# Optimization experiments

Hardware: AMD Instinct MI355X
Metric: run time of the kernel (lower is better)

## Reference

```python
import jax, jax.numpy as jnp
import numpy as np


def setup_inputs() -> dict:
    key = jax.random.key(0)
    k1, k2 = jax.random.split(key)
    B, N1, N2, D = 256, 32, 32, 512
    ner_j = jax.random.normal(k1, (B, N1, D), dtype=jnp.float32)
    face_j = jax.random.normal(k2, (B, N2, D), dtype=jnp.float32)
    return {"face_j": face_j, "ner_j": ner_j}


def reference(face_j, ner_j):
    # torch.matmul(ner_j.unsqueeze(1), face_j.permute(0,2,1)) broadcasts to the
    # pairwise score tensor: scores[b, c, n, f] = <ner_j[b, n], face_j[c, f]>
    scores = jnp.einsum('bnd,cfd->bcnf', ner_j, face_j)  # (B, B, N1, N2)
    # mean over num_spans2 then mean over num_spans1 (sum + div in original)
    logits = scores.mean(axis=-1).mean(axis=-1)           # (B, B)
    # cross_entropy(logits, targets=arange(B)) with mean reduction
    logp = jax.nn.log_softmax(logits, axis=-1)
    diag = jnp.diagonal(logp)                             # logp[b, b]
    return -jnp.mean(diag)
```

## Files before the change

kernel.cpp:

```cpp
#include <hip/hip_runtime.h>
#include <hip/hip_bf16.h>

#define BB 256
#define NN 32
#define DD 512
#define ROWS 2
#define KSPLIT 4

static __device__ inline unsigned f2bf(float x) {
  union { float f; unsigned u; } a; a.f = x;
  unsigned r = a.u + 0x7fff + ((a.u >> 16) & 1);
  return r >> 16;
}

__global__ __launch_bounds__(256) void reduce_sums(
    const float* __restrict__ ner, const float* __restrict__ face,
    float* __restrict__ u, unsigned* __restrict__ vTp, float* __restrict__ out) {
  int idx = blockIdx.x * 256 + threadIdx.x;
  if (idx == 0) out[0] = 0.0f;
  const int half = BB * DD / 4;
  bool is_ner = idx < half;
  int j = is_ner ? idx : idx - half;
  int row = j >> 7;
  int d4  = j & 127;
  const float* src = is_ner ? ner : face;
  const float4* p = (const float4*)(src + (size_t)row * NN * DD) + d4;
  float4 s = make_float4(0.f, 0.f, 0.f, 0.f);
#pragma unroll
  for (int n = 0; n < NN; ++n) {
    float4 x = p[n * (DD / 4)];
    s.x += x.x; s.y += x.y; s.z += x.z; s.w += x.w;
  }
  if (is_ner) {
    ((float4*)(u + (size_t)row * DD))[d4] = s;
  } else {
    int dp0 = 2 * d4;
    vTp[(size_t)dp0 * BB + row]       = (f2bf(s.y) << 16) | f2bf(s.x);
    vTp[(size_t)(dp0 + 1) * BB + row] = (f2bf(s.w) << 16) | f2bf(s.z);
  }
}

__global__ __launch_bounds__(1024) void row_lse_bf16(
    const float* __restrict__ u, const unsigned* __restrict__ vTp,
    float* __restrict__ out) {
  const int b0 = blockIdx.x * ROWS;
  const int t = threadIdx.x;
  const int c = t & 255;
  const int k = t >> 8;
  __shared__ float us[ROWS * DD];
  __shared__ float ls[KSPLIT][ROWS][BB];
  __shared__ float lg[ROWS][BB];
  __shared__ float wsum[ROWS];

  if (t < ROWS * DD / 4)
    ((float4*)us)[t] = ((const float4*)(u + (size_t)b0 * DD))[t];
  __syncthreads();

  float a0l = 0.f, a0h = 0.f, a1l = 0.f, a1h = 0.f;
  const unsigned* p = vTp + (size_t)(k * (DD / 2 / KSPLIT)) * BB + c;
  const float* u0 = us + k * (DD / KSPLIT);
  const float* u1 = us + DD + k * (DD / KSPLIT);
#pragma unroll 8
  for (int i = 0; i < DD / 2 / KSPLIT; ++i) {
    unsigned w = p[(size_t)i * BB];
    float vlo = __uint_as_float(w << 16);
    float vhi = __uint_as_float(w & 0xffff0000u);
    a0l = fmaf(u0[2 * i],     vlo, a0l);
    a0h = fmaf(u0[2 * i + 1], vhi, a0h);
    a1l = fmaf(u1[2 * i],     vlo, a1l);
    a1h = fmaf(u1[2 * i + 1], vhi, a1h);
  }
  ls[k][0][c] = a0l + a0h;
  ls[k][1][c] = a1l + a1h;
  __syncthreads();

  const float sc = 1.f / (NN * NN);
  if (t < ROWS * BB) {
    int cc = t & 255, r = t >> 8;
    lg[r][cc] = (ls[0][r][cc] + ls[1][r][cc] + ls[2][r][cc] + ls[3][r][cc]) * sc;
  }
  __syncthreads();

  const int wv = t >> 6, lane = t & 63;
  if (wv < ROWS) {
    float x0 = lg[wv][lane];
    float x1 = lg[wv][lane + 64];
    float x2 = lg[wv][lane + 128];
    float x3 = lg[wv][lane + 192];
    float m = fmaxf(fmaxf(x0, x1), fmaxf(x2, x3));
#pragma unroll
    for (int off = 32; off > 0; off >>= 1) m = fmaxf(m, __shfl_xor(m, off, 64));
    float e = __expf(x0 - m) + __expf(x1 - m) + __expf(x2 - m) + __expf(x3 - m);
#pragma unroll
    for (int off = 32; off > 0; off >>= 1) e += __shfl_xor(e, off, 64);
    if (lane == 0) wsum[wv] = lg[wv][b0 + wv] - (m + __logf(e));
  }
  __syncthreads();
  if (t == 0) atomicAdd(out, -(wsum[0] + wsum[1]) * (1.f / BB));
}

extern "C" void kernel_launch(void* const* d_in, const int* in_sizes, int n_in,
                              void* d_out, int out_size, void* d_ws, size_t ws_size,
                              hipStream_t stream) {
  const float* face = (const float*)d_in[0];
  const float* ner  = (const float*)d_in[1];
  float* u = (float*)d_ws;
  unsigned* vTp = (unsigned*)(u + (size_t)BB * DD);
  float* out = (float*)d_out;

  const int total_threads = 2 * BB * DD / 4;
  reduce_sums<<<total_threads / 256, 256, 0, stream>>>(ner, face, u, vTp, out);
  row_lse_bf16<<<BB / ROWS, 1024, 0, stream>>>(u, vTp, out);
}
```

Before: 80.00 us.

## Fuse span-sum and logsumexp kernels into one cooperative launch with grid sync

Merges the span-reduction kernel and the row log-softmax kernel into a single cooperative kernel of 256 blocks of 512 threads, with a grid-wide barrier between the phases. This removes one kernel launch and the dependency gap between them. The first phase now reduces float2 pairs per thread instead of float4, and the second phase computes one row per block with a 2-way K split instead of two rows per block with a 4-way split. The cost is the grid-sync overhead and less memory-level parallelism per thread in the reduction phase.

```diff
diff --git a/kernel.cpp b/kernel.cpp
--- a/kernel.cpp
+++ b/kernel.cpp
@@ -1,11 +1,12 @@
 #include <hip/hip_runtime.h>
-#include <hip/hip_bf16.h>
+#include <hip/hip_cooperative_groups.h>
+
+namespace cg = cooperative_groups;
 
 #define BB 256
 #define NN 32
 #define DD 512
-#define ROWS 2
-#define KSPLIT 4
+#define D2 (DD / 2)
 
 static __device__ inline unsigned f2bf(float x) {
   union { float f; unsigned u; } a; a.f = x;
@@ -13,90 +14,75 @@
   return r >> 16;
 }
 
-__global__ __launch_bounds__(256) void reduce_sums(
+__global__ __launch_bounds__(512) void fused_nce(
     const float* __restrict__ ner, const float* __restrict__ face,
-    float* __restrict__ u, unsigned* __restrict__ vTp, float* __restrict__ out) {
-  int idx = blockIdx.x * 256 + threadIdx.x;
-  if (idx == 0) out[0] = 0.0f;
-  const int half = BB * DD / 4;
-  bool is_ner = idx < half;
-  int j = is_ner ? idx : idx - half;
-  int row = j >> 7;
-  int d4  = j & 127;
-  const float* src = is_ner ? ner : face;
-  const float4* p = (const float4*)(src + (size_t)row * NN * DD) + d4;
-  float4 s = make_float4(0.f, 0.f, 0.f, 0.f);
+    float* __restrict__ u, unsigned* __restrict__ vTp,
+    float* __restrict__ out) {
+  const int t = threadIdx.x;
+  const int idx = blockIdx.x * 512 + t;
+
+  if (idx == 0) atomicExch(out, 0.0f);
+
+  {
+    const bool is_ner = idx < (BB * D2);
+    const int j = is_ner ? idx : idx - BB * D2;
+    const int row = j >> 8;
+    const int d2 = j & 255;
+    const float2* p =
+        (const float2*)(is_ner ? ner : face) + (size_t)row * (NN * D2) + d2;
+    float sx = 0.f, sy = 0.f;
 #pragma unroll
-  for (int n = 0; n < NN; ++n) {
-    float4 x = p[n * (DD / 4)];
-    s.x += x.x; s.y += x.y; s.z += x.z; s.w += x.w;
+    for (int n = 0; n < NN; ++n) {
+      float2 x = p[(size_t)n * D2];
+      sx += x.x; sy += x.y;
+    }
+    if (is_ner) {
+      ((float2*)u)[(size_t)row * D2 + d2] = make_float2(sx, sy);
+    } else {
+      vTp[(size_t)d2 * BB + row] = (f2bf(sy) << 16) | f2bf(sx);
+    }
   }
-  if (is_ner) {
-    ((float4*)(u + (size_t)row * DD))[d4] = s;
-  } else {
-    int dp0 = 2 * d4;
-    vTp[(size_t)dp0 * BB + row]       = (f2bf(s.y) << 16) | f2bf(s.x);
-    vTp[(size_t)(dp0 + 1) * BB + row] = (f2bf(s.w) << 16) | f2bf(s.z);
-  }
-}
 
-__global__ __launch_bounds__(1024) void row_lse_bf16(
-    const float* __restrict__ u, const unsigned* __restrict__ vTp,
-    float* __restrict__ out) {
-  const int b0 = blockIdx.x * ROWS;
-  const int t = threadIdx.x;
+  __threadfence();
+  cg::this_grid().sync();
+
+  const int b = blockIdx.x;
   const int c = t & 255;
   const int k = t >> 8;
-  __shared__ float us[ROWS * DD];
-  __shared__ float ls[KSPLIT][ROWS][BB];
-  __shared__ float lg[ROWS][BB];
-  __shared__ float wsum[ROWS];
+  __shared__ float us[DD];
+  __shared__ float ls[2][BB];
+  __shared__ float lg[BB];
 
-  if (t < ROWS * DD / 4)
-    ((float4*)us)[t] = ((const float4*)(u + (size_t)b0 * DD))[t];
+  us[t] = u[(size_t)b * DD + t];
   __syncthreads();
 
-  float a0l = 0.f, a0h = 0.f, a1l = 0.f, a1h = 0.f;
-  const unsigned* p = vTp + (size_t)(k * (DD / 2 / KSPLIT)) * BB + c;
-  const float* u0 = us + k * (DD / KSPLIT);
-  const float* u1 = us + DD + k * (DD / KSPLIT);
+  float al = 0.f, ah = 0.f;
+  const unsigned* p = vTp + (size_t)(k * (D2 / 2)) * BB + c;
+  const float* ub = us + k * (DD / 2);
 #pragma unroll 8
-  for (int i = 0; i < DD / 2 / KSPLIT; ++i) {
+  for (int i = 0; i < D2 / 2; ++i) {
     unsigned w = p[(size_t)i * BB];
     float vlo = __uint_as_float(w << 16);
     float vhi = __uint_as_float(w & 0xffff0000u);
-    a0l = fmaf(u0[2 * i],     vlo, a0l);
-    a0h = fmaf(u0[2 * i + 1], vhi, a0h);
-    a1l = fmaf(u1[2 * i],     vlo, a1l);
-    a1h = fmaf(u1[2 * i + 1], vhi, a1h);
+    al = fmaf(ub[2 * i],     vlo, al);
+    ah = fmaf(ub[2 * i + 1], vhi, ah);
   }
-  ls[k][0][c] = a0l + a0h;
-  ls[k][1][c] = a1l + a1h;
+  ls[k][c] = al + ah;
   __syncthreads();
 
-  const float sc = 1.f / (NN * NN);
-  if (t < ROWS * BB) {
-    int cc = t & 255, r = t >> 8;
-    lg[r][cc] = (ls[0][r][cc] + ls[1][r][cc] + ls[2][r][cc] + ls[3][r][cc]) * sc;
-  }
+  if (t < BB) lg[t] = (ls[0][t] + ls[1][t]) * (1.f / (NN * NN));
   __syncthreads();
 
-  const int wv = t >> 6, lane = t & 63;
-  if (wv < ROWS) {
-    float x0 = lg[wv][lane];
-    float x1 = lg[wv][lane + 64];
-    float x2 = lg[wv][lane + 128];
-    float x3 = lg[wv][lane + 192];
+  if (t < 64) {
+    float x0 = lg[t], x1 = lg[t + 64], x2 = lg[t + 128], x3 = lg[t + 192];
     float m = fmaxf(fmaxf(x0, x1), fmaxf(x2, x3));
 #pragma unroll
     for (int off = 32; off > 0; off >>= 1) m = fmaxf(m, __shfl_xor(m, off, 64));
     float e = __expf(x0 - m) + __expf(x1 - m) + __expf(x2 - m) + __expf(x3 - m);
 #pragma unroll
     for (int off = 32; off > 0; off >>= 1) e += __shfl_xor(e, off, 64);
-    if (lane == 0) wsum[wv] = lg[wv][b0 + wv] - (m + __logf(e));
+    if (t == 0) atomicAdd(out, -(lg[b] - (m + __logf(e))) * (1.f / BB));
   }
-  __syncthreads();
-  if (t == 0) atomicAdd(out, -(wsum[0] + wsum[1]) * (1.f / BB));
 }
 
 extern "C" void kernel_launch(void* const* d_in, const int* in_sizes, int n_in,
@@ -108,7 +94,7 @@
   unsigned* vTp = (unsigned*)(u + (size_t)BB * DD);
   float* out = (float*)d_out;
 
-  const int total_threads = 2 * BB * DD / 4;
-  reduce_sums<<<total_threads / 256, 256, 0, stream>>>(ner, face, u, vTp, out);
-  row_lse_bf16<<<BB / ROWS, 1024, 0, stream>>>(u, vTp, out);
+  void* args[] = {(void*)&ner, (void*)&face, (void*)&u, (void*)&vTp, (void*)&out};
+  hipLaunchCooperativeKernel(reinterpret_cast<void*>(fused_nce), dim3(BB),
+                             dim3(512), args, 0, stream);
 }
```

New measurement: 174.5 us. 118% more time.
